# Kernel optimization log

Measured on AMD Instinct MI355X. Metric: run time of the kernel, lower is better.

The kernel has to match this reference:

```python
import jax
jax.config.update("jax_enable_x64", True)  # torch code casts to double before exp; fp32 would overflow (exp up to ~e^333)
import jax.numpy as jnp
import numpy as np

SINKHORN_EPS = 0.003
SINKHORN_ITER = 50
MU = 0.25


def setup_inputs() -> dict:
    key = jax.random.key(0)
    k1, k2 = jax.random.split(key)
    x = jax.random.normal(k1, (8192, 512), dtype=jnp.float32)        # [B, D]
    codebook = jax.random.normal(k2, (8192, 512), dtype=jnp.float32)  # [K, D]
    return {"x": x, "codebook": codebook}


def _sinkhorn_assign(x, codebook):
    # squared euclidean distance: [B, K]
    d2 = (
        jnp.sum(x * x, axis=-1, keepdims=True)
        + jnp.sum(codebook * codebook, axis=-1)[None, :]
        - 2.0 * x @ codebook.T
    )
    max_d = d2.max()
    min_d = d2.min()
    mid_d = (max_d + min_d) / 2
    d2n = ((d2 - mid_d) / (max_d - mid_d + 1e-8)).astype(jnp.float64)
    M = jnp.exp(-d2n / SINKHORN_EPS)  # [B, K] float64
    B, K = M.shape
    M = M / M.sum()
    def body(_, M):
        M = M / (jnp.sum(M, axis=1, keepdims=True) + 1e-8) / B  # row normalize
        M = M / (jnp.sum(M, axis=0, keepdims=True) + 1e-8) / K  # col normalize
        return M
    M = jax.lax.fori_loop(0, SINKHORN_ITER, body, M)
    probs = M * B
    indices = jnp.argmax(probs, axis=-1)  # [B] int
    return probs, indices


def reference(x, codebook):
    probs, indices = _sinkhorn_assign(x, codebook)
    quant_hard = codebook[indices]  # [B, D]
    codebook_loss = jnp.mean((quant_hard - jax.lax.stop_gradient(x)) ** 2, axis=-1)
    commitment_loss = jnp.mean((jax.lax.stop_gradient(quant_hard) - x) ** 2, axis=-1)
    quant_soft = jax.lax.stop_gradient(quant_hard - x) + x  # straight-through
    loss = codebook_loss + MU * commitment_loss  # [B]
    return quant_hard, quant_soft, indices, probs, loss
```

## Files before the change

kernel.cpp:

```cpp
#include <hip/hip_runtime.h>
#include <math.h>

#define DD 512
#define NCH 64
#define BT 64
#define KC 16

struct Scal {
    unsigned maxbits, minbits;
    float mid, sc;
    double log2T;
};

__device__ __forceinline__ void onlineLSE(float& m, float& S, float t) {
    if (t <= m) {
        S += exp2f(t - m);
    } else {
        S = S * exp2f(m - t) + 1.0f;
        m = t;
    }
}

__device__ __forceinline__ void blockReduceMS(float& m, float& S, float* sm, float* ss) {
    int tid = threadIdx.x;
    sm[tid] = m; ss[tid] = S;
    __syncthreads();
    for (int s = 128; s > 0; s >>= 1) {
        if (tid < s) {
            float m2 = sm[tid + s], S2 = ss[tid + s];
            float m1 = sm[tid],     S1 = ss[tid];
            float nm = fmaxf(m1, m2);
            float nS;
            if (nm == -INFINITY) nS = 0.f;
            else nS = S1 * exp2f(m1 - nm) + S2 * exp2f(m2 - nm);
            sm[tid] = nm; ss[tid] = nS;
        }
        __syncthreads();
    }
    m = sm[0]; S = ss[0];
}

__global__ void k_init(Scal* s) {
    s->maxbits = 0u;
    s->minbits = 0xFFFFFFFFu;
}

__global__ void k_norms(const float* __restrict__ x, const float* __restrict__ cb,
                        float* __restrict__ xn, float* __restrict__ cn, int B) {
    int row = blockIdx.x;
    const float* src; float* dst; int r;
    if (row < B) { src = x + (size_t)row * DD; dst = xn; r = row; }
    else         { src = cb + (size_t)(row - B) * DD; dst = cn; r = row - B; }
    const float4* s4 = (const float4*)src;
    float s = 0.f;
    for (int q = threadIdx.x; q < DD / 4; q += 64) {
        float4 v = s4[q];
        s += v.x * v.x + v.y * v.y + v.z * v.z + v.w * v.w;
    }
    #pragma unroll
    for (int off = 32; off > 0; off >>= 1) s += __shfl_down(s, off, 64);
    if (threadIdx.x == 0) dst[r] = s;
}

__global__ __launch_bounds__(256) void k_gemm_d2(
        const float* __restrict__ x, const float* __restrict__ cb,
        const float* __restrict__ xn, const float* __restrict__ cn,
        float* __restrict__ d2, Scal* __restrict__ scal, int K) {
    __shared__ float As[KC][BT + 4];
    __shared__ float Bs[KC][BT + 4];
    int tid = threadIdx.x;
    int tx = tid & 15, ty = tid >> 4;
    int i0 = blockIdx.y * BT, j0 = blockIdx.x * BT;
    int lk = tid & 15, lrow = tid >> 4;
    float acc[4][4] = {};
    for (int k0 = 0; k0 < DD; k0 += KC) {
        __syncthreads();
        #pragma unroll
        for (int g = 0; g < 4; ++g) {
            As[lk][lrow + g * 16] = x [(size_t)(i0 + lrow + g * 16) * DD + k0 + lk];
            Bs[lk][lrow + g * 16] = cb[(size_t)(j0 + lrow + g * 16) * DD + k0 + lk];
        }
        __syncthreads();
        #pragma unroll
        for (int k = 0; k < KC; ++k) {
            float4 a4 = *(const float4*)&As[k][ty * 4];
            float4 b4 = *(const float4*)&Bs[k][tx * 4];
            float av[4] = {a4.x, a4.y, a4.z, a4.w};
            float bv[4] = {b4.x, b4.y, b4.z, b4.w};
            #pragma unroll
            for (int r = 0; r < 4; ++r)
                #pragma unroll
                for (int c = 0; c < 4; ++c)
                    acc[r][c] = fmaf(av[r], bv[c], acc[r][c]);
        }
    }
    float xr[4], cr[4];
    #pragma unroll
    for (int r = 0; r < 4; ++r) xr[r] = xn[i0 + ty * 4 + r];
    #pragma unroll
    for (int c = 0; c < 4; ++c) cr[c] = cn[j0 + tx * 4 + c];
    float lmax = -INFINITY, lmin = INFINITY;
    #pragma unroll
    for (int r = 0; r < 4; ++r) {
        float4 o;
        float* op = (float*)&o;
        #pragma unroll
        for (int c = 0; c < 4; ++c) {
            float v = (xr[r] + cr[c]) - 2.0f * acc[r][c];
            op[c] = v;
            lmax = fmaxf(lmax, v);
            lmin = fminf(lmin, v);
        }
        *(float4*)&d2[(size_t)(i0 + ty * 4 + r) * K + j0 + tx * 4] = o;
    }
    __shared__ float red[256];
    red[tid] = lmax; __syncthreads();
    for (int s = 128; s > 0; s >>= 1) { if (tid < s) red[tid] = fmaxf(red[tid], red[tid + s]); __syncthreads(); }
    if (tid == 0) atomicMax(&scal->maxbits, __float_as_uint(red[0]));
    __syncthreads();
    red[tid] = lmin; __syncthreads();
    for (int s = 128; s > 0; s >>= 1) { if (tid < s) red[tid] = fminf(red[tid], red[tid + s]); __syncthreads(); }
    if (tid == 0) atomicMin(&scal->minbits, __float_as_uint(red[0]));
}

__global__ void k_scalars(Scal* s) {
    float maxd = __uint_as_float(s->maxbits);
    float mind = __uint_as_float(s->minbits);
    float mid = (maxd + mind) * 0.5f;
    float den = (maxd - mid) + 1e-8f;
    s->mid = mid;
    s->sc = (float)(1.0 / ((double)den * 0.003 * 0.693147180559945309));
}

__global__ __launch_bounds__(256) void k_pass0_row(
        const float* __restrict__ d2, const Scal* __restrict__ scal,
        float* __restrict__ rowM, float* __restrict__ rowS, int K) {
    __shared__ float sm[256], ss[256];
    int i = blockIdx.x;
    float mid = scal->mid, sc = scal->sc;
    const float4* row = (const float4*)(d2 + (size_t)i * K);
    float m = -INFINITY, S = 0.f;
    for (int q = threadIdx.x; q < K / 4; q += 256) {
        float4 v = row[q];
        onlineLSE(m, S, (mid - v.x) * sc);
        onlineLSE(m, S, (mid - v.y) * sc);
        onlineLSE(m, S, (mid - v.z) * sc);
        onlineLSE(m, S, (mid - v.w) * sc);
    }
    blockReduceMS(m, S, sm, ss);
    if (threadIdx.x == 0) { rowM[i] = m; rowS[i] = S; }
}

__global__ void k_pass0_comb(const float* __restrict__ rowM, const float* __restrict__ rowS,
                             Scal* __restrict__ scal, int B) {
    __shared__ double sd[256];
    double acc = 0.0;
    for (int i = threadIdx.x; i < B; i += 256)
        acc += exp2((double)rowM[i]) * (double)rowS[i];
    sd[threadIdx.x] = acc; __syncthreads();
    for (int s = 128; s > 0; s >>= 1) { if (threadIdx.x < s) sd[threadIdx.x] += sd[threadIdx.x + s]; __syncthreads(); }
    if (threadIdx.x == 0) scal->log2T = log2(sd[0]);
}

__global__ void k_init_lrlc(double* __restrict__ lr2, float* __restrict__ lr2f,
                            double* __restrict__ lc2, float* __restrict__ lc2f,
                            const Scal* __restrict__ scal) {
    int i = blockIdx.x * 256 + threadIdx.x;
    double v = -scal->log2T;
    lr2[i] = v; lr2f[i] = (float)v;
    lc2[i] = 0.0; lc2f[i] = 0.f;
}

__global__ __launch_bounds__(256) void k_row_pass(
        const float* __restrict__ d2, const Scal* __restrict__ scal,
        const float* __restrict__ lc2f, double* __restrict__ lr2, float* __restrict__ lr2f,
        int K, double lg2B) {
    __shared__ float sm[256], ss[256];
    int i = blockIdx.x;
    float mid = scal->mid, sc = scal->sc;
    const float4* row = (const float4*)(d2 + (size_t)i * K);
    const float4* lc4 = (const float4*)lc2f;
    float m = -INFINITY, S = 0.f;
    for (int q = threadIdx.x; q < K / 4; q += 256) {
        float4 v = row[q];
        float4 l = lc4[q];
        onlineLSE(m, S, fmaf(mid - v.x, sc, l.x));
        onlineLSE(m, S, fmaf(mid - v.y, sc, l.y));
        onlineLSE(m, S, fmaf(mid - v.z, sc, l.z));
        onlineLSE(m, S, fmaf(mid - v.w, sc, l.w));
    }
    blockReduceMS(m, S, sm, ss);
    if (threadIdx.x == 0) {
        double lr = lr2[i];
        double rowsum = exp2(lr + (double)m) * (double)S;
        double nlr = lr - log2(rowsum + 1e-8) - lg2B;
        lr2[i] = nlr; lr2f[i] = (float)nlr;
    }
}

__global__ __launch_bounds__(256) void k_col_pass(
        const float* __restrict__ d2, const Scal* __restrict__ scal,
        const float* __restrict__ lr2f, float* __restrict__ colM, float* __restrict__ colS,
        int B, int K) {
    int jj = (blockIdx.x * 256 + threadIdx.x) * 2;
    int ch = blockIdx.y;
    int i0 = ch * (B / NCH), i1 = i0 + B / NCH;
    float mid = scal->mid, sc = scal->sc;
    float m0 = -INFINITY, S0 = 0.f, m1 = -INFINITY, S1 = 0.f;
    for (int i = i0; i < i1; ++i) {
        float lr = lr2f[i];
        float2 v = *(const float2*)&d2[(size_t)i * K + jj];
        onlineLSE(m0, S0, fmaf(mid - v.x, sc, lr));
        onlineLSE(m1, S1, fmaf(mid - v.y, sc, lr));
    }
    size_t o = (size_t)ch * K + jj;
    *(float2*)&colM[o] = make_float2(m0, m1);
    *(float2*)&colS[o] = make_float2(S0, S1);
}

__global__ void k_col_comb(const float* __restrict__ colM, const float* __restrict__ colS,
                           double* __restrict__ lc2, float* __restrict__ lc2f,
                           int K, double lg2K) {
    int j = blockIdx.x * 256 + threadIdx.x;
    float m = -INFINITY, S = 0.f;
    for (int ch = 0; ch < NCH; ++ch) {
        float m2 = colM[(size_t)ch * K + j], S2 = colS[(size_t)ch * K + j];
        if (m2 <= m) S += S2 * exp2f(m2 - m);
        else { S = S * exp2f(m - m2) + S2; m = m2; }
    }
    double lc = lc2[j];
    double colsum = exp2(lc + (double)m) * (double)S;
    double nlc = lc - log2(colsum + 1e-8) - lg2K;
    lc2[j] = nlc; lc2f[j] = (float)nlc;
}

__global__ __launch_bounds__(256) void k_final(
        float* __restrict__ d2probs, const Scal* __restrict__ scal,
        const double* __restrict__ lr2, const float* __restrict__ lc2f,
        float* __restrict__ oidx, int K, float lg2B) {
    __shared__ float sv[256];
    __shared__ int sj[256];
    int i = blockIdx.x;
    float mid = scal->mid, sc = scal->sc;
    float rb = (float)lr2[i] + lg2B;
    float4* row = (float4*)(d2probs + (size_t)i * K);
    const float4* lc4 = (const float4*)lc2f;
    float bt = -INFINITY; int bj = 0;
    for (int q = threadIdx.x; q < K / 4; q += 256) {
        float4 v = row[q];
        float4 l = lc4[q];
        float t0 = fmaf(mid - v.x, sc, rb + l.x);
        float t1 = fmaf(mid - v.y, sc, rb + l.y);
        float t2 = fmaf(mid - v.z, sc, rb + l.z);
        float t3 = fmaf(mid - v.w, sc, rb + l.w);
        row[q] = make_float4(exp2f(t0), exp2f(t1), exp2f(t2), exp2f(t3));
        int j0 = q * 4;
        if (t0 > bt) { bt = t0; bj = j0; }
        if (t1 > bt) { bt = t1; bj = j0 + 1; }
        if (t2 > bt) { bt = t2; bj = j0 + 2; }
        if (t3 > bt) { bt = t3; bj = j0 + 3; }
    }
    sv[threadIdx.x] = bt; sj[threadIdx.x] = bj;
    __syncthreads();
    for (int s = 128; s > 0; s >>= 1) {
        if (threadIdx.x < s) {
            float v2 = sv[threadIdx.x + s]; int j2 = sj[threadIdx.x + s];
            if (v2 > sv[threadIdx.x] || (v2 == sv[threadIdx.x] && j2 < sj[threadIdx.x])) {
                sv[threadIdx.x] = v2; sj[threadIdx.x] = j2;
            }
        }
        __syncthreads();
    }
    if (threadIdx.x == 0) oidx[i] = (float)sj[0];
}

__global__ __launch_bounds__(128) void k_epilogue(
        const float* __restrict__ x, const float* __restrict__ cb,
        const float* __restrict__ oidx, float* __restrict__ qh, float* __restrict__ qs,
        float* __restrict__ loss) {
    __shared__ float sw[2];
    int i = blockIdx.x;
    int idx = (int)oidx[i];
    const float4* cr  = (const float4*)(cb + (size_t)idx * DD);
    const float4* xr  = (const float4*)(x + (size_t)i * DD);
    float4* qhr = (float4*)(qh + (size_t)i * DD);
    float4* qsr = (float4*)(qs + (size_t)i * DD);
    float acc = 0.f;
    for (int q = threadIdx.x; q < DD / 4; q += 128) {
        float4 c = cr[q], xv = xr[q];
        qhr[q] = c;
        float dx = c.x - xv.x, dy = c.y - xv.y, dz = c.z - xv.z, dw = c.w - xv.w;
        qsr[q] = make_float4(dx + xv.x, dy + xv.y, dz + xv.z, dw + xv.w);
        acc += dx * dx + dy * dy + dz * dz + dw * dw;
    }
    #pragma unroll
    for (int off = 32; off > 0; off >>= 1) acc += __shfl_down(acc, off, 64);
    if ((threadIdx.x & 63) == 0) sw[threadIdx.x >> 6] = acc;
    __syncthreads();
    if (threadIdx.x == 0) loss[i] = 1.25f * ((sw[0] + sw[1]) / 512.f);
}

extern "C" void kernel_launch(void* const* d_in, const int* in_sizes, int n_in,
                              void* d_out, int out_size, void* d_ws, size_t ws_size,
                              hipStream_t stream) {
    (void)n_in; (void)out_size; (void)d_ws; (void)ws_size;
    const float* x  = (const float*)d_in[0];
    const float* cb = (const float*)d_in[1];
    int B = in_sizes[0] / DD;
    int K = in_sizes[1] / DD;

    float* out   = (float*)d_out;
    float* qh    = out;
    float* qs    = qh + (size_t)B * DD;
    float* oidx  = qs + (size_t)B * DD;
    float* probs = oidx + B;
    float* loss  = probs + (size_t)B * K;

    char* p = (char*)qs;
    double* lr2  = (double*)p; p += (size_t)B * 8;
    double* lc2  = (double*)p; p += (size_t)K * 8;
    float*  lr2f = (float*)p;  p += (size_t)B * 4;
    float*  lc2f = (float*)p;  p += (size_t)K * 4;
    float*  rowM = (float*)p;  p += (size_t)B * 4;
    float*  rowS = (float*)p;  p += (size_t)B * 4;
    float*  xn   = (float*)p;  p += (size_t)B * 4;
    float*  cn   = (float*)p;  p += (size_t)K * 4;
    float*  colM = (float*)p;  p += (size_t)NCH * K * 4;
    float*  colS = (float*)p;  p += (size_t)NCH * K * 4;
    Scal*   scal = (Scal*)p;

    double lg2B = log2((double)B), lg2K = log2((double)K);

    k_init<<<1, 1, 0, stream>>>(scal);
    k_norms<<<B + K, 64, 0, stream>>>(x, cb, xn, cn, B);
    k_gemm_d2<<<dim3(K / BT, B / BT), 256, 0, stream>>>(x, cb, xn, cn, probs, scal, K);
    k_scalars<<<1, 1, 0, stream>>>(scal);
    k_pass0_row<<<B, 256, 0, stream>>>(probs, scal, rowM, rowS, K);
    k_pass0_comb<<<1, 256, 0, stream>>>(rowM, rowS, scal, B);
    k_init_lrlc<<<B / 256, 256, 0, stream>>>(lr2, lr2f, lc2, lc2f, scal);
    for (int it = 0; it < 50; ++it) {
        k_row_pass<<<B, 256, 0, stream>>>(probs, scal, lc2f, lr2, lr2f, K, lg2B);
        k_col_pass<<<dim3(K / 512, NCH), 256, 0, stream>>>(probs, scal, lr2f, colM, colS, B, K);
        k_col_comb<<<K / 256, 256, 0, stream>>>(colM, colS, lc2, lc2f, K, lg2K);
    }
    k_final<<<B, 256, 0, stream>>>(probs, scal, lr2, lc2f, oidx, K, (float)lg2B);
    k_epilogue<<<B, 128, 0, stream>>>(x, cb, oidx, qh, qs, loss);
}
```

Baseline: 8.452 ms.

## Fuse Sinkhorn row and column passes into one kernel reading d2 once

```diff
diff --git a/kernel.cpp b/kernel.cpp
--- a/kernel.cpp
+++ b/kernel.cpp
@@ -2,7 +2,6 @@
 #include <math.h>
 
 #define DD 512
-#define NCH 64
 #define BT 64
 #define KC 16
 
@@ -19,6 +18,11 @@
         S = S * exp2f(m - t) + 1.0f;
         m = t;
     }
+}
+
+__device__ __forceinline__ void mergeMS(float& m, float& S, float m2, float S2) {
+    if (m2 <= m) S += S2 * exp2f(m2 - m);
+    else { S = S * exp2f(m - m2) + S2; m = m2; }
 }
 
 __device__ __forceinline__ void blockReduceMS(float& m, float& S, float* sm, float* ss) {
@@ -171,65 +175,101 @@
     lc2[i] = 0.0; lc2f[i] = 0.f;
 }
 
-__global__ __launch_bounds__(256) void k_row_pass(
+__global__ __launch_bounds__(256, 1) void k_iter_fused(
         const float* __restrict__ d2, const Scal* __restrict__ scal,
         const float* __restrict__ lc2f, double* __restrict__ lr2, float* __restrict__ lr2f,
-        int K, double lg2B) {
-    __shared__ float sm[256], ss[256];
-    int i = blockIdx.x;
+        float* __restrict__ colM, float* __restrict__ colS,
+        int K, int RCH, double lg2B) {
+    __shared__ float lds_lc[8192];
+    __shared__ float redM[4], redS[4];
+    __shared__ float bc;
+    int tid = threadIdx.x;
     float mid = scal->mid, sc = scal->sc;
-    const float4* row = (const float4*)(d2 + (size_t)i * K);
-    const float4* lc4 = (const float4*)lc2f;
-    float m = -INFINITY, S = 0.f;
-    for (int q = threadIdx.x; q < K / 4; q += 256) {
-        float4 v = row[q];
-        float4 l = lc4[q];
-        onlineLSE(m, S, fmaf(mid - v.x, sc, l.x));
-        onlineLSE(m, S, fmaf(mid - v.y, sc, l.y));
-        onlineLSE(m, S, fmaf(mid - v.z, sc, l.z));
-        onlineLSE(m, S, fmaf(mid - v.w, sc, l.w));
-    }
-    blockReduceMS(m, S, sm, ss);
-    if (threadIdx.x == 0) {
-        double lr = lr2[i];
-        double rowsum = exp2(lr + (double)m) * (double)S;
-        double nlr = lr - log2(rowsum + 1e-8) - lg2B;
-        lr2[i] = nlr; lr2f[i] = (float)nlr;
-    }
-}
-
-__global__ __launch_bounds__(256) void k_col_pass(
-        const float* __restrict__ d2, const Scal* __restrict__ scal,
-        const float* __restrict__ lr2f, float* __restrict__ colM, float* __restrict__ colS,
-        int B, int K) {
-    int jj = (blockIdx.x * 256 + threadIdx.x) * 2;
-    int ch = blockIdx.y;
-    int i0 = ch * (B / NCH), i1 = i0 + B / NCH;
-    float mid = scal->mid, sc = scal->sc;
-    float m0 = -INFINITY, S0 = 0.f, m1 = -INFINITY, S1 = 0.f;
-    for (int i = i0; i < i1; ++i) {
-        float lr = lr2f[i];
-        float2 v = *(const float2*)&d2[(size_t)i * K + jj];
-        onlineLSE(m0, S0, fmaf(mid - v.x, sc, lr));
-        onlineLSE(m1, S1, fmaf(mid - v.y, sc, lr));
-    }
-    size_t o = (size_t)ch * K + jj;
-    *(float2*)&colM[o] = make_float2(m0, m1);
-    *(float2*)&colS[o] = make_float2(S0, S1);
+    #pragma unroll
+    for (int k = 0; k < 8; ++k) {
+        int q = tid + (k << 8);
+        ((float4*)lds_lc)[q] = ((const float4*)lc2f)[q];
+    }
+    float mC[32], SC[32];
+    #pragma unroll
+    for (int e = 0; e < 32; ++e) { mC[e] = -INFINITY; SC[e] = 0.f; }
+    __syncthreads();
+    int i0 = blockIdx.x * RCH;
+    for (int r = 0; r < RCH; ++r) {
+        int i = i0 + r;
+        const float4* row = (const float4*)(d2 + (size_t)i * K);
+        float s2c[32];
+        float m0 = -INFINITY, m1 = -INFINITY, m2 = -INFINITY, m3 = -INFINITY;
+        float S0 = 0.f, S1 = 0.f, S2 = 0.f, S3 = 0.f;
+        #pragma unroll
+        for (int k = 0; k < 8; ++k) {
+            int q = tid + (k << 8);
+            float4 v = row[q];
+            float4 l = ((const float4*)lds_lc)[q];
+            float t0 = (mid - v.x) * sc;
+            float t1 = (mid - v.y) * sc;
+            float t2 = (mid - v.z) * sc;
+            float t3 = (mid - v.w) * sc;
+            s2c[k * 4 + 0] = t0; s2c[k * 4 + 1] = t1;
+            s2c[k * 4 + 2] = t2; s2c[k * 4 + 3] = t3;
+            onlineLSE(m0, S0, t0 + l.x);
+            onlineLSE(m1, S1, t1 + l.y);
+            onlineLSE(m2, S2, t2 + l.z);
+            onlineLSE(m3, S3, t3 + l.w);
+        }
+        mergeMS(m0, S0, m1, S1);
+        mergeMS(m2, S2, m3, S3);
+        mergeMS(m0, S0, m2, S2);
+        #pragma unroll
+        for (int off = 32; off > 0; off >>= 1) {
+            float mo = __shfl_xor(m0, off, 64);
+            float So = __shfl_xor(S0, off, 64);
+            mergeMS(m0, S0, mo, So);
+        }
+        if ((tid & 63) == 0) { redM[tid >> 6] = m0; redS[tid >> 6] = S0; }
+        __syncthreads();
+        if (tid == 0) {
+            float mm = redM[0], SS = redS[0];
+            mergeMS(mm, SS, redM[1], redS[1]);
+            mergeMS(mm, SS, redM[2], redS[2]);
+            mergeMS(mm, SS, redM[3], redS[3]);
+            double lr = lr2[i];
+            double rowsum = exp2(lr + (double)mm) * (double)SS;
+            double nlr = lr - log2(rowsum + 1e-8) - lg2B;
+            lr2[i] = nlr; lr2f[i] = (float)nlr;
+            bc = (float)nlr;
+        }
+        __syncthreads();
+        float lrN = bc;
+        #pragma unroll
+        for (int e = 0; e < 32; ++e) onlineLSE(mC[e], SC[e], s2c[e] + lrN);
+    }
+    size_t o = (size_t)blockIdx.x * K;
+    #pragma unroll
+    for (int k = 0; k < 8; ++k) {
+        int q = tid + (k << 8);
+        *(float4*)&colM[o + q * 4] = make_float4(mC[k*4], mC[k*4+1], mC[k*4+2], mC[k*4+3]);
+        *(float4*)&colS[o + q * 4] = make_float4(SC[k*4], SC[k*4+1], SC[k*4+2], SC[k*4+3]);
+    }
 }
 
 __global__ void k_col_comb(const float* __restrict__ colM, const float* __restrict__ colS,
                            double* __restrict__ lc2, float* __restrict__ lc2f,
-                           int K, double lg2K) {
+                           int K, int NCH, double lg2K) {
     int j = blockIdx.x * 256 + threadIdx.x;
-    float m = -INFINITY, S = 0.f;
-    for (int ch = 0; ch < NCH; ++ch) {
-        float m2 = colM[(size_t)ch * K + j], S2 = colS[(size_t)ch * K + j];
-        if (m2 <= m) S += S2 * exp2f(m2 - m);
-        else { S = S * exp2f(m - m2) + S2; m = m2; }
-    }
+    float m0 = -INFINITY, S0 = 0.f, m1 = -INFINITY, S1 = 0.f;
+    float m2 = -INFINITY, S2 = 0.f, m3 = -INFINITY, S3 = 0.f;
+    for (int ch = 0; ch < NCH; ch += 4) {
+        mergeMS(m0, S0, colM[(size_t)ch * K + j],       colS[(size_t)ch * K + j]);
+        mergeMS(m1, S1, colM[(size_t)(ch + 1) * K + j], colS[(size_t)(ch + 1) * K + j]);
+        mergeMS(m2, S2, colM[(size_t)(ch + 2) * K + j], colS[(size_t)(ch + 2) * K + j]);
+        mergeMS(m3, S3, colM[(size_t)(ch + 3) * K + j], colS[(size_t)(ch + 3) * K + j]);
+    }
+    mergeMS(m0, S0, m1, S1);
+    mergeMS(m2, S2, m3, S3);
+    mergeMS(m0, S0, m2, S2);
     double lc = lc2[j];
-    double colsum = exp2(lc + (double)m) * (double)S;
+    double colsum = exp2(lc + (double)m0) * (double)S0;
     double nlc = lc - log2(colsum + 1e-8) - lg2K;
     lc2[j] = nlc; lc2f[j] = (float)nlc;
 }
@@ -303,7 +343,7 @@
 extern "C" void kernel_launch(void* const* d_in, const int* in_sizes, int n_in,
                               void* d_out, int out_size, void* d_ws, size_t ws_size,
                               hipStream_t stream) {
-    (void)n_in; (void)out_size; (void)d_ws; (void)ws_size;
+    (void)n_in; (void)out_size;
     const float* x  = (const float*)d_in[0];
     const float* cb = (const float*)d_in[1];
     int B = in_sizes[0] / DD;
@@ -325,9 +365,20 @@
     float*  rowS = (float*)p;  p += (size_t)B * 4;
     float*  xn   = (float*)p;  p += (size_t)B * 4;
     float*  cn   = (float*)p;  p += (size_t)K * 4;
-    float*  colM = (float*)p;  p += (size_t)NCH * K * 4;
-    float*  colS = (float*)p;  p += (size_t)NCH * K * 4;
-    Scal*   scal = (Scal*)p;
+    Scal*   scal = (Scal*)p;   p += 256;
+
+    int NCH; float *colM, *colS;
+    size_t need512 = (size_t)512 * K * 4 * 2;
+    if (ws_size >= need512) {
+        NCH = 512;
+        colM = (float*)d_ws;
+        colS = colM + (size_t)512 * K;
+    } else {
+        NCH = 128;
+        colM = (float*)p;
+        colS = colM + (size_t)128 * K;
+    }
+    int RCH = B / NCH;
 
     double lg2B = log2((double)B), lg2K = log2((double)K);
 
@@ -339,9 +390,9 @@
     k_pass0_comb<<<1, 256, 0, stream>>>(rowM, rowS, scal, B);
     k_init_lrlc<<<B / 256, 256, 0, stream>>>(lr2, lr2f, lc2, lc2f, scal);
     for (int it = 0; it < 50; ++it) {
-        k_row_pass<<<B, 256, 0, stream>>>(probs, scal, lc2f, lr2, lr2f, K, lg2B);
-        k_col_pass<<<dim3(K / 512, NCH), 256, 0, stream>>>(probs, scal, lr2f, colM, colS, B, K);
-        k_col_comb<<<K / 256, 256, 0, stream>>>(colM, colS, lc2, lc2f, K, lg2K);
+        k_iter_fused<<<NCH, 256, 0, stream>>>(probs, scal, lc2f, lr2, lr2f,
+                                              colM, colS, K, RCH, lg2B);
+        k_col_comb<<<K / 256, 256, 0, stream>>>(colM, colS, lc2, lc2f, K, NCH, lg2K);
     }
     k_final<<<B, 256, 0, stream>>>(probs, scal, lr2, lc2f, oidx, K, (float)lg2B);
     k_epilogue<<<B, 128, 0, stream>>>(x, cb, oidx, qh, qs, loss);
```

After: 19.49 ms. 2.31x slower.

## Enlarge GEMM tiles, add ILP to Sinkhorn row/col passes

Applied to the files above, without the earlier changes.

```diff
diff --git a/kernel.cpp b/kernel.cpp
--- a/kernel.cpp
+++ b/kernel.cpp
@@ -2,8 +2,8 @@
 #include <math.h>
 
 #define DD 512
-#define NCH 64
-#define BT 64
+#define NCH 128
+#define BT 128
 #define KC 16
 
 struct Scal {
@@ -19,6 +19,11 @@
         S = S * exp2f(m - t) + 1.0f;
         m = t;
     }
+}
+
+__device__ __forceinline__ void mergeMS(float& m, float& S, float m2, float S2) {
+    if (m2 <= m) S += S2 * exp2f(m2 - m);
+    else { S = S * exp2f(m - m2) + S2; m = m2; }
 }
 
 __device__ __forceinline__ void blockReduceMS(float& m, float& S, float* sm, float* ss) {
@@ -72,46 +77,49 @@
     int tx = tid & 15, ty = tid >> 4;
     int i0 = blockIdx.y * BT, j0 = blockIdx.x * BT;
     int lk = tid & 15, lrow = tid >> 4;
-    float acc[4][4] = {};
+    float acc[8][8] = {};
     for (int k0 = 0; k0 < DD; k0 += KC) {
         __syncthreads();
         #pragma unroll
-        for (int g = 0; g < 4; ++g) {
+        for (int g = 0; g < 8; ++g) {
             As[lk][lrow + g * 16] = x [(size_t)(i0 + lrow + g * 16) * DD + k0 + lk];
             Bs[lk][lrow + g * 16] = cb[(size_t)(j0 + lrow + g * 16) * DD + k0 + lk];
         }
         __syncthreads();
         #pragma unroll
         for (int k = 0; k < KC; ++k) {
-            float4 a4 = *(const float4*)&As[k][ty * 4];
-            float4 b4 = *(const float4*)&Bs[k][tx * 4];
-            float av[4] = {a4.x, a4.y, a4.z, a4.w};
-            float bv[4] = {b4.x, b4.y, b4.z, b4.w};
+            float4 a0 = *(const float4*)&As[k][ty * 8];
+            float4 a1 = *(const float4*)&As[k][ty * 8 + 4];
+            float4 b0 = *(const float4*)&Bs[k][tx * 8];
+            float4 b1 = *(const float4*)&Bs[k][tx * 8 + 4];
+            float av[8] = {a0.x, a0.y, a0.z, a0.w, a1.x, a1.y, a1.z, a1.w};
+            float bv[8] = {b0.x, b0.y, b0.z, b0.w, b1.x, b1.y, b1.z, b1.w};
             #pragma unroll
-            for (int r = 0; r < 4; ++r)
+            for (int r = 0; r < 8; ++r)
                 #pragma unroll
-                for (int c = 0; c < 4; ++c)
+                for (int c = 0; c < 8; ++c)
                     acc[r][c] = fmaf(av[r], bv[c], acc[r][c]);
         }
     }
-    float xr[4], cr[4];
-    #pragma unroll
-    for (int r = 0; r < 4; ++r) xr[r] = xn[i0 + ty * 4 + r];
-    #pragma unroll
-    for (int c = 0; c < 4; ++c) cr[c] = cn[j0 + tx * 4 + c];
+    float xr[8], cr[8];
+    #pragma unroll
+    for (int r = 0; r < 8; ++r) xr[r] = xn[i0 + ty * 8 + r];
+    #pragma unroll
+    for (int c = 0; c < 8; ++c) cr[c] = cn[j0 + tx * 8 + c];
     float lmax = -INFINITY, lmin = INFINITY;
     #pragma unroll
-    for (int r = 0; r < 4; ++r) {
-        float4 o;
-        float* op = (float*)&o;
+    for (int r = 0; r < 8; ++r) {
+        float o[8];
         #pragma unroll
-        for (int c = 0; c < 4; ++c) {
+        for (int c = 0; c < 8; ++c) {
             float v = (xr[r] + cr[c]) - 2.0f * acc[r][c];
-            op[c] = v;
+            o[c] = v;
             lmax = fmaxf(lmax, v);
             lmin = fminf(lmin, v);
         }
-        *(float4*)&d2[(size_t)(i0 + ty * 4 + r) * K + j0 + tx * 4] = o;
+        float* dst = &d2[(size_t)(i0 + ty * 8 + r) * K + j0 + tx * 8];
+        *(float4*)dst       = make_float4(o[0], o[1], o[2], o[3]);
+        *(float4*)(dst + 4) = make_float4(o[4], o[5], o[6], o[7]);
     }
     __shared__ float red[256];
     red[tid] = lmax; __syncthreads();
@@ -180,19 +188,32 @@
     float mid = scal->mid, sc = scal->sc;
     const float4* row = (const float4*)(d2 + (size_t)i * K);
     const float4* lc4 = (const float4*)lc2f;
-    float m = -INFINITY, S = 0.f;
-    for (int q = threadIdx.x; q < K / 4; q += 256) {
-        float4 v = row[q];
-        float4 l = lc4[q];
-        onlineLSE(m, S, fmaf(mid - v.x, sc, l.x));
-        onlineLSE(m, S, fmaf(mid - v.y, sc, l.y));
-        onlineLSE(m, S, fmaf(mid - v.z, sc, l.z));
-        onlineLSE(m, S, fmaf(mid - v.w, sc, l.w));
-    }
-    blockReduceMS(m, S, sm, ss);
+    float m[8], S[8];
+    #pragma unroll
+    for (int t = 0; t < 8; ++t) { m[t] = -INFINITY; S[t] = 0.f; }
+    for (int q = threadIdx.x; q < K / 8; q += 256) {
+        float4 va = row[q * 2],  vb = row[q * 2 + 1];
+        float4 la = lc4[q * 2],  lb = lc4[q * 2 + 1];
+        onlineLSE(m[0], S[0], fmaf(mid - va.x, sc, la.x));
+        onlineLSE(m[1], S[1], fmaf(mid - va.y, sc, la.y));
+        onlineLSE(m[2], S[2], fmaf(mid - va.z, sc, la.z));
+        onlineLSE(m[3], S[3], fmaf(mid - va.w, sc, la.w));
+        onlineLSE(m[4], S[4], fmaf(mid - vb.x, sc, lb.x));
+        onlineLSE(m[5], S[5], fmaf(mid - vb.y, sc, lb.y));
+        onlineLSE(m[6], S[6], fmaf(mid - vb.z, sc, lb.z));
+        onlineLSE(m[7], S[7], fmaf(mid - vb.w, sc, lb.w));
+    }
+    mergeMS(m[0], S[0], m[1], S[1]);
+    mergeMS(m[2], S[2], m[3], S[3]);
+    mergeMS(m[4], S[4], m[5], S[5]);
+    mergeMS(m[6], S[6], m[7], S[7]);
+    mergeMS(m[0], S[0], m[2], S[2]);
+    mergeMS(m[4], S[4], m[6], S[6]);
+    mergeMS(m[0], S[0], m[4], S[4]);
+    blockReduceMS(m[0], S[0], sm, ss);
     if (threadIdx.x == 0) {
         double lr = lr2[i];
-        double rowsum = exp2(lr + (double)m) * (double)S;
+        double rowsum = exp2(lr + (double)m[0]) * (double)S[0];
         double nlr = lr - log2(rowsum + 1e-8) - lg2B;
         lr2[i] = nlr; lr2f[i] = (float)nlr;
     }
@@ -202,34 +223,43 @@
         const float* __restrict__ d2, const Scal* __restrict__ scal,
         const float* __restrict__ lr2f, float* __restrict__ colM, float* __restrict__ colS,
         int B, int K) {
-    int jj = (blockIdx.x * 256 + threadIdx.x) * 2;
+    int j0 = (blockIdx.x * 256 + threadIdx.x) * 4;
     int ch = blockIdx.y;
     int i0 = ch * (B / NCH), i1 = i0 + B / NCH;
     float mid = scal->mid, sc = scal->sc;
-    float m0 = -INFINITY, S0 = 0.f, m1 = -INFINITY, S1 = 0.f;
+    float m[4], S[4];
+    #pragma unroll
+    for (int t = 0; t < 4; ++t) { m[t] = -INFINITY; S[t] = 0.f; }
     for (int i = i0; i < i1; ++i) {
         float lr = lr2f[i];
-        float2 v = *(const float2*)&d2[(size_t)i * K + jj];
-        onlineLSE(m0, S0, fmaf(mid - v.x, sc, lr));
-        onlineLSE(m1, S1, fmaf(mid - v.y, sc, lr));
-    }
-    size_t o = (size_t)ch * K + jj;
-    *(float2*)&colM[o] = make_float2(m0, m1);
-    *(float2*)&colS[o] = make_float2(S0, S1);
+        float4 v = *(const float4*)&d2[(size_t)i * K + j0];
+        onlineLSE(m[0], S[0], fmaf(mid - v.x, sc, lr));
+        onlineLSE(m[1], S[1], fmaf(mid - v.y, sc, lr));
+        onlineLSE(m[2], S[2], fmaf(mid - v.z, sc, lr));
+        onlineLSE(m[3], S[3], fmaf(mid - v.w, sc, lr));
+    }
+    size_t o = (size_t)ch * K + j0;
+    *(float4*)&colM[o] = make_float4(m[0], m[1], m[2], m[3]);
+    *(float4*)&colS[o] = make_float4(S[0], S[1], S[2], S[3]);
 }
 
 __global__ void k_col_comb(const float* __restrict__ colM, const float* __restrict__ colS,
                            double* __restrict__ lc2, float* __restrict__ lc2f,
                            int K, double lg2K) {
     int j = blockIdx.x * 256 + threadIdx.x;
-    float m = -INFINITY, S = 0.f;
-    for (int ch = 0; ch < NCH; ++ch) {
-        float m2 = colM[(size_t)ch * K + j], S2 = colS[(size_t)ch * K + j];
-        if (m2 <= m) S += S2 * exp2f(m2 - m);
-        else { S = S * exp2f(m - m2) + S2; m = m2; }
-    }
+    float m0 = -INFINITY, S0 = 0.f, m1 = -INFINITY, S1 = 0.f;
+    float m2 = -INFINITY, S2 = 0.f, m3 = -INFINITY, S3 = 0.f;
+    for (int ch = 0; ch < NCH; ch += 4) {
+        mergeMS(m0, S0, colM[(size_t)ch * K + j],       colS[(size_t)ch * K + j]);
+        mergeMS(m1, S1, colM[(size_t)(ch + 1) * K + j], colS[(size_t)(ch + 1) * K + j]);
+        mergeMS(m2, S2, colM[(size_t)(ch + 2) * K + j], colS[(size_t)(ch + 2) * K + j]);
+        mergeMS(m3, S3, colM[(size_t)(ch + 3) * K + j], colS[(size_t)(ch + 3) * K + j]);
+    }
+    mergeMS(m0, S0, m1, S1);
+    mergeMS(m2, S2, m3, S3);
+    mergeMS(m0, S0, m2, S2);
     double lc = lc2[j];
-    double colsum = exp2(lc + (double)m) * (double)S;
+    double colsum = exp2(lc + (double)m0) * (double)S0;
     double nlc = lc - log2(colsum + 1e-8) - lg2K;
     lc2[j] = nlc; lc2f[j] = (float)nlc;
 }
@@ -325,9 +355,9 @@
     float*  rowS = (float*)p;  p += (size_t)B * 4;
     float*  xn   = (float*)p;  p += (size_t)B * 4;
     float*  cn   = (float*)p;  p += (size_t)K * 4;
+    Scal*   scal = (Scal*)p;   p += 256;
     float*  colM = (float*)p;  p += (size_t)NCH * K * 4;
-    float*  colS = (float*)p;  p += (size_t)NCH * K * 4;
-    Scal*   scal = (Scal*)p;
+    float*  colS = (float*)p;
 
     double lg2B = log2((double)B), lg2K = log2((double)K);
 
@@ -340,7 +370,7 @@
     k_init_lrlc<<<B / 256, 256, 0, stream>>>(lr2, lr2f, lc2, lc2f, scal);
     for (int it = 0; it < 50; ++it) {
         k_row_pass<<<B, 256, 0, stream>>>(probs, scal, lc2f, lr2, lr2f, K, lg2B);
-        k_col_pass<<<dim3(K / 512, NCH), 256, 0, stream>>>(probs, scal, lr2f, colM, colS, B, K);
+        k_col_pass<<<dim3(K / 1024, NCH), 256, 0, stream>>>(probs, scal, lr2f, colM, colS, B, K);
         k_col_comb<<<K / 256, 256, 0, stream>>>(colM, colS, lc2, lc2f, K, lg2K);
     }
     k_final<<<B, 256, 0, stream>>>(probs, scal, lr2, lc2f, oidx, K, (float)lg2B);
```

New measurement: 8.964 ms. 1.06x slower.
